# Optimization experiments

Measured on AMD Instinct MI355X. Metric: run time of the kernel, lower is better.

Reference implementation:

```python
import jax, jax.numpy as jnp
import numpy as np

EPS = 1e-3  # Keras BatchNormalization default epsilon
HEADS = 4
KEY_DEPTH = 16   # k
INTRA = 1        # u
VAL_DEPTH = 64   # v = kernel_out // heads = 256 // 4
C_IN = 256
B, HH, WW = 16, 32, 32
N = HH * WW      # == size of positional embedding


def setup_inputs() -> dict:
    key = jax.random.key(0)
    ks = jax.random.split(key, 6)
    x = jax.random.normal(ks[0], (B, HH, WW, C_IN), dtype=jnp.float32)
    # 1x1 conv kernels == dense matrices over the channel dim
    Wq = jax.random.normal(ks[1], (C_IN, KEY_DEPTH * HEADS), dtype=jnp.float32) * 0.05
    Wk = jax.random.normal(ks[2], (C_IN, KEY_DEPTH * INTRA), dtype=jnp.float32) * 0.05
    Wv = jax.random.normal(ks[3], (C_IN, VAL_DEPTH * INTRA), dtype=jnp.float32) * 0.05
    # BatchNorm (inference mode) parameters
    gamma_q = jnp.ones((KEY_DEPTH * HEADS,), jnp.float32)
    beta_q = jnp.zeros((KEY_DEPTH * HEADS,), jnp.float32)
    mean_q = jnp.zeros((KEY_DEPTH * HEADS,), jnp.float32)
    var_q = jnp.ones((KEY_DEPTH * HEADS,), jnp.float32)
    gamma_v = jnp.ones((VAL_DEPTH * INTRA,), jnp.float32)
    beta_v = jnp.zeros((VAL_DEPTH * INTRA,), jnp.float32)
    mean_v = jnp.zeros((VAL_DEPTH * INTRA,), jnp.float32)
    var_v = jnp.ones((VAL_DEPTH * INTRA,), jnp.float32)
    # Positional embedding: [size, size, key_depth, intra_depth], uniform init
    E = jax.random.uniform(ks[4], (N, N, KEY_DEPTH, INTRA), dtype=jnp.float32)
    return {
        'x': x, 'Wq': Wq, 'Wk': Wk, 'Wv': Wv,
        'gamma_q': gamma_q, 'beta_q': beta_q, 'mean_q': mean_q, 'var_q': var_q,
        'gamma_v': gamma_v, 'beta_v': beta_v, 'mean_v': mean_v, 'var_v': var_v,
        'E': E,
    }


def _bn(t, gamma, beta, mean, var):
    return gamma * (t - mean) / jnp.sqrt(var + EPS) + beta


def reference(x, Wq, Wk, Wv, gamma_q, beta_q, mean_q, var_q,
              gamma_v, beta_v, mean_v, var_v, E):
    b, hh, ww, _ = x.shape
    n = hh * ww
    # 1x1 conv projections (context c == x)
    q = jnp.einsum('bhwc,cd->bhwd', x, Wq)           # [b,hh,ww,h*k]
    k = jnp.einsum('bhwc,cd->bhwd', x, Wk)           # [b,hh,ww,u*k]
    v = jnp.einsum('bhwc,cd->bhwd', x, Wv)           # [b,hh,ww,u*v]
    q = _bn(q, gamma_q, beta_q, mean_q, var_q)
    v = _bn(v, gamma_v, beta_v, mean_v, var_v)
    # softmax over the channel axis (faithful to the source code)
    k = jax.nn.softmax(k, axis=-1)
    # rearranges: b hh ww (h k) -> b h k n ; b hh ww (u k) -> b u k n ; b hh ww (u v) -> b u v n
    q = q.reshape(b, n, HEADS, KEY_DEPTH).transpose(0, 2, 3, 1)   # [b,h,k,n]
    k = k.reshape(b, n, INTRA, KEY_DEPTH).transpose(0, 2, 3, 1)   # [b,u,k,n]
    v = v.reshape(b, n, INTRA, VAL_DEPTH).transpose(0, 2, 3, 1)   # [b,u,v,n]
    # content lambda: sum over intra-depth and positions
    lam_c = jnp.einsum('bukn,buvn->bkv', k, v)                    # [b,k,v]
    Yc = jnp.einsum('bhkn,bkv->bhvn', q, lam_c)                   # [b,h,v,n]
    # positional lambdas: E[n,m,k,u] contracted with v[b,u,v,m]
    lam_p = jnp.einsum('nmku,buvm->bnkv', E, v)                   # [b,n,k,v]
    Yp = jnp.einsum('bhkn,bnkv->bhvn', q, lam_p)                  # [b,h,v,n]
    Y = Yc + Yp                                                    # [b,h,v,n]
    # b h v n -> b hh ww (h v)
    out = Y.transpose(0, 3, 1, 2).reshape(b, hh, ww, HEADS * VAL_DEPTH)
    return out
```

## Files before the change

### kernel.cpp

```cpp
#include <hip/hip_runtime.h>
#include <stdint.h>

#define EPS 1e-3f

typedef __bf16 bf16x8 __attribute__((ext_vector_type(8)));
typedef float  f32x4  __attribute__((ext_vector_type(4)));

static __device__ __forceinline__ uint16_t f2bf(float f) {
  union { float f; uint32_t u; } v; v.f = f;
  uint32_t u = v.u;
  uint32_t r = u + 0x7fffu + ((u >> 16) & 1u);
  return (uint16_t)(r >> 16);
}
static __device__ __forceinline__ uint32_t pack2bf(float lo, float hi) {
  union { uint16_t h[2]; uint32_t u; } r;
  r.h[0] = f2bf(lo); r.h[1] = f2bf(hi);
  return r.u;
}
static __device__ __forceinline__ void gload_lds16(const void* g, void* l) {
  __builtin_amdgcn_global_load_lds(
      (const __attribute__((address_space(1))) unsigned int*)g,
      (__attribute__((address_space(3))) unsigned int*)l, 16, 0, 0);
}

__global__ __launch_bounds__(256) void wprep(
    const float* __restrict__ Wq, const float* __restrict__ Wk,
    const float* __restrict__ Wv, uint16_t* __restrict__ WtP)
{
  const int col = blockIdx.x, t = threadIdx.x;
  float val = (col < 64) ? Wq[t * 64 + col]
            : (col < 80) ? Wk[t * 16 + (col - 64)]
                         : Wv[t * 64 + (col - 80)];
  WtP[col * 264 + t] = f2bf(val);
}

__global__ __launch_bounds__(256) void proj_mfma(
    const float* __restrict__ x, const uint16_t* __restrict__ WtP,
    const float* __restrict__ gq, const float* __restrict__ bq,
    const float* __restrict__ mq, const float* __restrict__ vq,
    const float* __restrict__ gv, const float* __restrict__ bv,
    const float* __restrict__ mv, const float* __restrict__ vvp,
    float* __restrict__ Qf, uint16_t* __restrict__ VbfT,
    float* __restrict__ part)
{
  __shared__ __align__(16) char smem[111616];
  uint16_t* const xA = (uint16_t*)smem;
  char* const Wt = smem + 33792;

  const int t = threadIdx.x;
  const int wid = t >> 6, lane = t & 63;
  const int bid = blockIdx.x;
  const int b = bid >> 4, mc = bid & 15;
  const int r0 = b * 1024 + mc * 64;

#pragma unroll
  for (int i = 0; i < 19; ++i) {
    int off = (i * 256 + t) * 16;
    gload_lds16((const char*)WtP + off, Wt + off);
  }
  {
    const int row = t >> 2, ks0 = (t & 3) * 64;
    const float* src = x + (size_t)(r0 + row) * 256 + ks0;
    uint16_t* dstp = xA + row * 264 + ks0;
#pragma unroll
    for (int i = 0; i < 8; ++i) {
      float4 d0 = *(const float4*)(src + i * 8);
      float4 d1 = *(const float4*)(src + i * 8 + 4);
      union { uint16_t u[8]; uint4 q; } pk;
      pk.u[0] = f2bf(d0.x); pk.u[1] = f2bf(d0.y);
      pk.u[2] = f2bf(d0.z); pk.u[3] = f2bf(d0.w);
      pk.u[4] = f2bf(d1.x); pk.u[5] = f2bf(d1.y);
      pk.u[6] = f2bf(d1.z); pk.u[7] = f2bf(d1.w);
      *(uint4*)(dstp + i * 8) = pk.q;
    }
  }
  __syncthreads();

  f32x4 acc[9];
#pragma unroll
  for (int f = 0; f < 9; ++f) acc[f] = f32x4{0.f, 0.f, 0.f, 0.f};
  const int arow = wid * 16 + (lane & 15);
#pragma unroll
  for (int kst = 0; kst < 8; ++kst) {
    const int sb = kst * 64 + ((lane >> 4) << 4);
    bf16x8 af = *(const bf16x8*)((const char*)xA + arow * 528 + sb);
#pragma unroll
    for (int f = 0; f < 9; ++f) {
      const int crow = f * 16 + (lane & 15);
      bf16x8 bfr = *(const bf16x8*)(Wt + crow * 528 + sb);
      acc[f] = __builtin_amdgcn_mfma_f32_16x16x32_bf16(af, bfr, acc[f], 0, 0, 0);
    }
  }

  const int cl = lane & 15;
  const int rbase = wid * 16 + ((lane >> 4) << 2);

  float qs[4], qb[4], qm[4], vs[4], vb[4], vm[4];
#pragma unroll
  for (int f = 0; f < 4; ++f) {
    const int c = f * 16 + cl;
    qs[f] = gq[c] * rsqrtf(vq[c] + EPS); qb[f] = bq[c]; qm[f] = mq[c];
    vs[f] = gv[c] * rsqrtf(vvp[c] + EPS); vb[f] = bv[c]; vm[f] = mv[c];
  }
#pragma unroll
  for (int f = 0; f < 4; ++f)
#pragma unroll
    for (int r = 0; r < 4; ++r)
      Qf[(size_t)(r0 + rbase + r) * 64 + f * 16 + cl] =
          (acc[f][r] - qm[f]) * qs[f] + qb[f];
  float ex[4];
#pragma unroll
  for (int r = 0; r < 4; ++r) {
    float kv = acc[4][r];
    float mx = kv;
#pragma unroll
    for (int d = 1; d < 16; d <<= 1) mx = fmaxf(mx, __shfl_xor(mx, d, 64));
    float e = __expf(kv - mx);
    float sm = e;
#pragma unroll
    for (int d = 1; d < 16; d <<= 1) sm += __shfl_xor(sm, d, 64);
    ex[r] = e / sm;
  }
  float vv[4][4];
#pragma unroll
  for (int f = 0; f < 4; ++f)
#pragma unroll
    for (int r = 0; r < 4; ++r)
      vv[f][r] = (acc[5 + f][r] - vm[f]) * vs[f] + vb[f];

  __syncthreads();
  float* const vt = (float*)smem;
  float* const ks = (float*)(smem + 64 * 65 * 4);
#pragma unroll
  for (int r = 0; r < 4; ++r) ks[(rbase + r) * 20 + cl] = ex[r];
#pragma unroll
  for (int f = 0; f < 4; ++f)
#pragma unroll
    for (int r = 0; r < 4; ++r) vt[(rbase + r) * 65 + f * 16 + cl] = vv[f][r];
  __syncthreads();

  {
    const int v = t & 63, grp = t >> 6;
#pragma unroll
    for (int h = 0; h < 2; ++h) {
      union { uint16_t u16[8]; uint4 q; } pk;
#pragma unroll
      for (int i = 0; i < 8; ++i)
        pk.u16[i] = f2bf(vt[(grp * 16 + h * 8 + i) * 65 + v]);
      *(uint4*)&VbfT[(size_t)(b * 64 + v) * 1024 + mc * 64 + grp * 16 + h * 8] = pk.q;
    }
  }
  {
    const int kq = t >> 6, v = t & 63;
    float a0 = 0.f, a1 = 0.f, a2 = 0.f, a3 = 0.f;
#pragma unroll 4
    for (int m = 0; m < 64; ++m) {
      float vvx = vt[m * 65 + v];
      a0 = fmaf(ks[m * 20 + kq * 4 + 0], vvx, a0);
      a1 = fmaf(ks[m * 20 + kq * 4 + 1], vvx, a1);
      a2 = fmaf(ks[m * 20 + kq * 4 + 2], vvx, a2);
      a3 = fmaf(ks[m * 20 + kq * 4 + 3], vvx, a3);
    }
    float* dst = part + ((size_t)(b * 16 + mc) << 10) + (kq * 4) * 64 + v;
    dst[0] = a0; dst[64] = a1; dst[128] = a2; dst[192] = a3;
  }
}

__global__ __launch_bounds__(256) void lamc_reduce(const float* __restrict__ part,
                                                   float* __restrict__ Lc)
{
  const int gid = blockIdx.x * 256 + threadIdx.x;
  const int b = gid >> 10, r = gid & 1023;
  const float* p = part + ((size_t)b << 14) + r;
  float s = 0.f;
#pragma unroll
  for (int mc = 0; mc < 16; ++mc) s += p[mc << 10];
  Lc[((size_t)b << 10) + r] = s;
}

__global__ __launch_bounds__(256, 2) void gemm_out(
    const float* __restrict__ E,
    const uint16_t* __restrict__ VbfT,
    const float* __restrict__ Qf,
    const float* __restrict__ Lc,
    float* __restrict__ out)
{
  __shared__ __align__(16) char smem[65536];
  char* const A0 = smem;
  char* const B0 = smem + 16384;
  char* const A1 = smem + 32768;
  char* const B1 = smem + 49152;

  const int t = threadIdx.x;
  const int wid = t >> 6, lane = t & 63;
  const int wm = wid >> 1, wn = wid & 1;
  const int bid = blockIdx.x;
  const int xcd = bid & 7, idx = bid >> 3;
  const int rb = xcd * 16 + (idx >> 3);
  const int cb = idx & 7;
  const int col0 = cb * 128;
  const int n0 = rb * 8;

  const int kq = t & 3;
  const int mp = (t >> 2) & 31;
  const int nb = t >> 7;
  const float* Eb = E + ((size_t)n0 << 14);

  int awoff[4][4];
#pragma unroll
  for (int it = 0; it < 4; ++it)
#pragma unroll
    for (int j = 0; j < 4; ++j) {
      int row = (it * 2 + nb) * 16 + kq * 4 + j;
      awoff[it][j] = row * 128 + ((mp * 4) ^ ((row & 7) << 4));
    }

  const uint16_t* bptr[4];
  int bdst[4];
  {
    const uint16_t* Bb = VbfT + ((size_t)col0 << 10);
#pragma unroll
    for (int it = 0; it < 4; ++it) {
      int id = it * 256 + t;
      int row = id >> 3, seg = id & 7;
      bptr[it] = Bb + (row << 10) + ((seg ^ (row & 7)) << 3);
      bdst[it] = id * 16;
    }
  }

  f32x4 acc[4][4];
#pragma unroll
  for (int i = 0; i < 4; ++i)
#pragma unroll
    for (int j = 0; j < 4; ++j) acc[i][j] = f32x4{0.f, 0.f, 0.f, 0.f};

  float4 ra[4], rbx[4];

#pragma unroll
  for (int it = 0; it < 4; ++it) {
    size_t base = ((size_t)(it * 2 + nb) << 14) + ((size_t)(mp * 2) << 4) + (kq << 2);
    ra[it]  = *(const float4*)(Eb + base);
    rbx[it] = *(const float4*)(Eb + base + 16);
  }
#pragma unroll
  for (int it = 0; it < 4; ++it) gload_lds16(bptr[it], B0 + bdst[it]);
#pragma unroll
  for (int it = 0; it < 4; ++it) {
    const float* da = (const float*)&ra[it];
    const float* db = (const float*)&rbx[it];
#pragma unroll
    for (int j = 0; j < 4; ++j)
      *(uint32_t*)(A0 + awoff[it][j]) = pack2bf(da[j], db[j]);
  }
  __syncthreads();

#pragma unroll 1
  for (int kt = 0; kt < 16; ++kt) {
    char* Ac = (kt & 1) ? A1 : A0;
    char* Bc = (kt & 1) ? B1 : B0;
    char* An = (kt & 1) ? A0 : A1;
    char* Bn = (kt & 1) ? B0 : B1;
    if (kt < 15) {
      const int m0n = (kt + 1) * 64;
#pragma unroll
      for (int it = 0; it < 4; ++it) {
        size_t base = ((size_t)(it * 2 + nb) << 14) +
                      ((size_t)(m0n + mp * 2) << 4) + (kq << 2);
        ra[it]  = *(const float4*)(Eb + base);
        rbx[it] = *(const float4*)(Eb + base + 16);
      }
#pragma unroll
      for (int it = 0; it < 4; ++it) gload_lds16(bptr[it] + m0n, Bn + bdst[it]);
    }
    __builtin_amdgcn_s_setprio(1);
#pragma unroll
    for (int kk = 0; kk < 2; ++kk) {
      bf16x8 a[4], b[4];
      const int s = kk * 4 + (lane >> 4);
#pragma unroll
      for (int i = 0; i < 4; ++i) {
        int row = wm * 64 + i * 16 + (lane & 15);
        a[i] = *(const bf16x8*)(Ac + row * 128 + ((s ^ (row & 7)) << 4));
      }
#pragma unroll
      for (int j = 0; j < 4; ++j) {
        int row = wn * 64 + j * 16 + (lane & 15);
        b[j] = *(const bf16x8*)(Bc + row * 128 + ((s ^ (row & 7)) << 4));
      }
#pragma unroll
      for (int i = 0; i < 4; ++i)
#pragma unroll
        for (int j = 0; j < 4; ++j)
          acc[i][j] = __builtin_amdgcn_mfma_f32_16x16x32_bf16(a[i], b[j], acc[i][j], 0, 0, 0);
    }
    __builtin_amdgcn_s_setprio(0);
    if (kt < 15) {
#pragma unroll
      for (int it = 0; it < 4; ++it) {
        const float* da = (const float*)&ra[it];
        const float* db = (const float*)&rbx[it];
#pragma unroll
        for (int j = 0; j < 4; ++j)
          *(uint32_t*)(An + awoff[it][j]) = pack2bf(da[j], db[j]);
      }
    }
    __syncthreads();
  }

  float* Cs = (float*)smem;
  const int b0 = cb * 2;
#pragma unroll
  for (int p = 0; p < 2; ++p) {
    if (wm == p) {
#pragma unroll
      for (int i = 0; i < 4; ++i) {
#pragma unroll
        for (int j = 0; j < 4; ++j) {
          const int col = wn * 64 + j * 16 + (lane & 15);
          const int bb = b0 + (col >> 6), v = col & 63;
#pragma unroll
          for (int r = 0; r < 4; ++r) {
            const int rl = i * 16 + ((lane >> 4) << 2) + r;
            const int k = rl & 15;
            Cs[rl * 132 + col] = acc[i][j][r] + Lc[(size_t)(((bb << 4) + k) << 6) + v];
          }
        }
      }
    }
    __syncthreads();
    {
      const int v = t & 63, g = t >> 6;
#pragma unroll
      for (int c = 0; c < 8; ++c) {
        const int combo = g + (c << 2);
        const int n_l = combo >> 3;
        const int b_l = (combo >> 2) & 1;
        const int h = combo & 3;
        const int n = n0 + (p << 2) + n_l;
        const int bb = b0 + b_l;
        const float* qp = Qf + (((size_t)(bb << 10) + n) << 6) + (h << 4);
        float sum = 0.f;
#pragma unroll
        for (int k = 0; k < 16; ++k)
          sum = fmaf(qp[k], Cs[((n_l << 4) + k) * 132 + (b_l << 6) + v], sum);
        out[(((size_t)(bb << 10) + n) << 8) + (h << 6) + v] = sum;
      }
    }
    __syncthreads();
  }
}

extern "C" void kernel_launch(void* const* d_in, const int* in_sizes, int n_in,
                              void* d_out, int out_size, void* d_ws, size_t ws_size,
                              hipStream_t stream) {
  const float* x   = (const float*)d_in[0];
  const float* Wq  = (const float*)d_in[1];
  const float* Wk  = (const float*)d_in[2];
  const float* Wv  = (const float*)d_in[3];
  const float* gq  = (const float*)d_in[4];
  const float* bq  = (const float*)d_in[5];
  const float* mq  = (const float*)d_in[6];
  const float* vq  = (const float*)d_in[7];
  const float* gv  = (const float*)d_in[8];
  const float* bv  = (const float*)d_in[9];
  const float* mv  = (const float*)d_in[10];
  const float* vvp = (const float*)d_in[11];
  const float* E   = (const float*)d_in[12];
  float* out = (float*)d_out;

  char* ws = (char*)d_ws;
  uint16_t* VbfT = (uint16_t*)(ws);
  float*    Qf   = (float*)(ws + (size_t)(2 << 20));
  float*    part = (float*)(ws + (size_t)(6 << 20));
  float*    Lc   = (float*)(ws + (size_t)(7 << 20));
  uint16_t* WtP  = (uint16_t*)(ws + (size_t)(7 << 20) + 65536);

  hipLaunchKernelGGL(wprep, dim3(144), dim3(256), 0, stream, Wq, Wk, Wv, WtP);
  hipLaunchKernelGGL(proj_mfma, dim3(256), dim3(256), 0, stream, x, WtP,
                     gq, bq, mq, vq, gv, bv, mv, vvp, Qf, VbfT, part);
  hipLaunchKernelGGL(lamc_reduce, dim3(64), dim3(256), 0, stream, part, Lc);
  hipLaunchKernelGGL(gemm_out, dim3(1024), dim3(256), 0, stream, E, VbfT, Qf, Lc, out);
}
```

Measured before the change: 82.56 us.

## Restructure E tile loading to 8 m-rows per thread, preload Lc into accumulators

The gemm_out E-tile load is remapped so each thread reads 8 consecutive m rows for one n and k-quad and writes one 16-byte packed bf16 store per row, instead of many 4-byte LDS stores. The content-lambda Lc is used as the initial accumulator value rather than added in the epilogue. Float-to-bf16 conversion switches from manual bit rounding to native __bf16 casts. The LDS buffer order is also swapped. The intent is fewer LDS write instructions and less ALU work, at the cost of a different global access pattern for E.

```diff
diff --git a/kernel.cpp b/kernel.cpp
--- a/kernel.cpp
+++ b/kernel.cpp
@@ -7,14 +7,11 @@
 typedef float  f32x4  __attribute__((ext_vector_type(4)));
 
 static __device__ __forceinline__ uint16_t f2bf(float f) {
-  union { float f; uint32_t u; } v; v.f = f;
-  uint32_t u = v.u;
-  uint32_t r = u + 0x7fffu + ((u >> 16) & 1u);
-  return (uint16_t)(r >> 16);
-}
-static __device__ __forceinline__ uint32_t pack2bf(float lo, float hi) {
-  union { uint16_t h[2]; uint32_t u; } r;
-  r.h[0] = f2bf(lo); r.h[1] = f2bf(hi);
+  union { __bf16 b; uint16_t u; } r; r.b = (__bf16)f; return r.u;
+}
+static __device__ __forceinline__ uint32_t cvt2(float lo, float hi) {
+  union { __bf16 b[2]; uint32_t u; } r;
+  r.b[0] = (__bf16)lo; r.b[1] = (__bf16)hi;
   return r.u;
 }
 static __device__ __forceinline__ void gload_lds16(const void* g, void* l) {
@@ -66,12 +63,10 @@
     for (int i = 0; i < 8; ++i) {
       float4 d0 = *(const float4*)(src + i * 8);
       float4 d1 = *(const float4*)(src + i * 8 + 4);
-      union { uint16_t u[8]; uint4 q; } pk;
-      pk.u[0] = f2bf(d0.x); pk.u[1] = f2bf(d0.y);
-      pk.u[2] = f2bf(d0.z); pk.u[3] = f2bf(d0.w);
-      pk.u[4] = f2bf(d1.x); pk.u[5] = f2bf(d1.y);
-      pk.u[6] = f2bf(d1.z); pk.u[7] = f2bf(d1.w);
-      *(uint4*)(dstp + i * 8) = pk.q;
+      uint4 q;
+      q.x = cvt2(d0.x, d0.y); q.y = cvt2(d0.z, d0.w);
+      q.z = cvt2(d1.x, d1.y); q.w = cvt2(d1.z, d1.w);
+      *(uint4*)(dstp + i * 8) = q;
     }
   }
   __syncthreads();
@@ -143,11 +138,12 @@
     const int v = t & 63, grp = t >> 6;
 #pragma unroll
     for (int h = 0; h < 2; ++h) {
-      union { uint16_t u16[8]; uint4 q; } pk;
-#pragma unroll
-      for (int i = 0; i < 8; ++i)
-        pk.u16[i] = f2bf(vt[(grp * 16 + h * 8 + i) * 65 + v]);
-      *(uint4*)&VbfT[(size_t)(b * 64 + v) * 1024 + mc * 64 + grp * 16 + h * 8] = pk.q;
+      uint4 q;
+      q.x = cvt2(vt[(grp * 16 + h * 8 + 0) * 65 + v], vt[(grp * 16 + h * 8 + 1) * 65 + v]);
+      q.y = cvt2(vt[(grp * 16 + h * 8 + 2) * 65 + v], vt[(grp * 16 + h * 8 + 3) * 65 + v]);
+      q.z = cvt2(vt[(grp * 16 + h * 8 + 4) * 65 + v], vt[(grp * 16 + h * 8 + 5) * 65 + v]);
+      q.w = cvt2(vt[(grp * 16 + h * 8 + 6) * 65 + v], vt[(grp * 16 + h * 8 + 7) * 65 + v]);
+      *(uint4*)&VbfT[(size_t)(b * 64 + v) * 1024 + mc * 64 + grp * 16 + h * 8] = q;
     }
   }
   {
@@ -187,8 +183,8 @@
 {
   __shared__ __align__(16) char smem[65536];
   char* const A0 = smem;
-  char* const B0 = smem + 16384;
-  char* const A1 = smem + 32768;
+  char* const A1 = smem + 16384;
+  char* const B0 = smem + 32768;
   char* const B1 = smem + 49152;
 
   const int t = threadIdx.x;
@@ -200,20 +196,19 @@
   const int cb = idx & 7;
   const int col0 = cb * 128;
   const int n0 = rb * 8;
+  const int b0i = cb * 2;
 
   const int kq = t & 3;
-  const int mp = (t >> 2) & 31;
-  const int nb = t >> 7;
-  const float* Eb = E + ((size_t)n0 << 14);
-
-  int awoff[4][4];
-#pragma unroll
-  for (int it = 0; it < 4; ++it)
-#pragma unroll
-    for (int j = 0; j < 4; ++j) {
-      int row = (it * 2 + nb) * 16 + kq * 4 + j;
-      awoff[it][j] = row * 128 + ((mp * 4) ^ ((row & 7) << 4));
-    }
+  const int mp = (t >> 2) & 7;
+  const int nl = t >> 5;
+  const float* Eb = E + ((size_t)(n0 + nl) << 14) + (size_t)(mp * 8) * 16 + kq * 4;
+
+  int awoff[4];
+#pragma unroll
+  for (int j = 0; j < 4; ++j) {
+    int row = nl * 16 + kq * 4 + j;
+    awoff[j] = row * 128 + ((mp ^ (row & 7)) << 4);
+  }
 
   const uint16_t* bptr[4];
   int bdst[4];
@@ -229,28 +224,34 @@
   }
 
   f32x4 acc[4][4];
-#pragma unroll
-  for (int i = 0; i < 4; ++i)
-#pragma unroll
-    for (int j = 0; j < 4; ++j) acc[i][j] = f32x4{0.f, 0.f, 0.f, 0.f};
-
-  float4 ra[4], rbx[4];
-
-#pragma unroll
-  for (int it = 0; it < 4; ++it) {
-    size_t base = ((size_t)(it * 2 + nb) << 14) + ((size_t)(mp * 2) << 4) + (kq << 2);
-    ra[it]  = *(const float4*)(Eb + base);
-    rbx[it] = *(const float4*)(Eb + base + 16);
-  }
+  {
+#pragma unroll
+    for (int j = 0; j < 4; ++j) {
+      const int col = wn * 64 + j * 16 + (lane & 15);
+      const int bb = b0i + (col >> 6), v = col & 63;
+      const float* lp = Lc + (size_t)(((bb << 4) + ((lane >> 4) << 2)) << 6) + v;
+      f32x4 lc;
+#pragma unroll
+      for (int r = 0; r < 4; ++r) lc[r] = lp[r << 6];
+#pragma unroll
+      for (int i = 0; i < 4; ++i) acc[i][j] = lc;
+    }
+  }
+
+  float4 ef[8];
+
+#pragma unroll
+  for (int mm = 0; mm < 8; ++mm) ef[mm] = *(const float4*)(Eb + mm * 16);
 #pragma unroll
   for (int it = 0; it < 4; ++it) gload_lds16(bptr[it], B0 + bdst[it]);
 #pragma unroll
-  for (int it = 0; it < 4; ++it) {
-    const float* da = (const float*)&ra[it];
-    const float* db = (const float*)&rbx[it];
-#pragma unroll
-    for (int j = 0; j < 4; ++j)
-      *(uint32_t*)(A0 + awoff[it][j]) = pack2bf(da[j], db[j]);
+  for (int j = 0; j < 4; ++j) {
+    uint4 w;
+    w.x = cvt2(((const float*)&ef[0])[j], ((const float*)&ef[1])[j]);
+    w.y = cvt2(((const float*)&ef[2])[j], ((const float*)&ef[3])[j]);
+    w.z = cvt2(((const float*)&ef[4])[j], ((const float*)&ef[5])[j]);
+    w.w = cvt2(((const float*)&ef[6])[j], ((const float*)&ef[7])[j]);
+    *(uint4*)(A0 + awoff[j]) = w;
   }
   __syncthreads();
 
@@ -263,12 +264,8 @@
     if (kt < 15) {
       const int m0n = (kt + 1) * 64;
 #pragma unroll
-      for (int it = 0; it < 4; ++it) {
-        size_t base = ((size_t)(it * 2 + nb) << 14) +
-                      ((size_t)(m0n + mp * 2) << 4) + (kq << 2);
-        ra[it]  = *(const float4*)(Eb + base);
-        rbx[it] = *(const float4*)(Eb + base + 16);
-      }
+      for (int mm = 0; mm < 8; ++mm)
+        ef[mm] = *(const float4*)(Eb + (size_t)(m0n + mm) * 16);
 #pragma unroll
       for (int it = 0; it < 4; ++it) gload_lds16(bptr[it] + m0n, Bn + bdst[it]);
     }
@@ -296,19 +293,19 @@
     __builtin_amdgcn_s_setprio(0);
     if (kt < 15) {
 #pragma unroll
-      for (int it = 0; it < 4; ++it) {
-        const float* da = (const float*)&ra[it];
-        const float* db = (const float*)&rbx[it];
-#pragma unroll
-        for (int j = 0; j < 4; ++j)
-          *(uint32_t*)(An + awoff[it][j]) = pack2bf(da[j], db[j]);
+      for (int j = 0; j < 4; ++j) {
+        uint4 w;
+        w.x = cvt2(((const float*)&ef[0])[j], ((const float*)&ef[1])[j]);
+        w.y = cvt2(((const float*)&ef[2])[j], ((const float*)&ef[3])[j]);
+        w.z = cvt2(((const float*)&ef[4])[j], ((const float*)&ef[5])[j]);
+        w.w = cvt2(((const float*)&ef[6])[j], ((const float*)&ef[7])[j]);
+        *(uint4*)(An + awoff[j]) = w;
       }
     }
     __syncthreads();
   }
 
   float* Cs = (float*)smem;
-  const int b0 = cb * 2;
 #pragma unroll
   for (int p = 0; p < 2; ++p) {
     if (wm == p) {
@@ -317,12 +314,10 @@
 #pragma unroll
         for (int j = 0; j < 4; ++j) {
           const int col = wn * 64 + j * 16 + (lane & 15);
-          const int bb = b0 + (col >> 6), v = col & 63;
 #pragma unroll
           for (int r = 0; r < 4; ++r) {
             const int rl = i * 16 + ((lane >> 4) << 2) + r;
-            const int k = rl & 15;
-            Cs[rl * 132 + col] = acc[i][j][r] + Lc[(size_t)(((bb << 4) + k) << 6) + v];
+            Cs[rl * 132 + col] = acc[i][j][r];
           }
         }
       }
@@ -337,7 +332,7 @@
         const int b_l = (combo >> 2) & 1;
         const int h = combo & 3;
         const int n = n0 + (p << 2) + n_l;
-        const int bb = b0 + b_l;
+        const int bb = b0i + b_l;
         const float* qp = Qf + (((size_t)(bb << 10) + n) << 6) + (h << 4);
         float sum = 0.f;
 #pragma unroll
```

After: 85.68 us. 3.8% more time.
